# Optimization experiments

Measured on AMD Instinct MI355X. Metric: run time of the kernel, lower is better.

## Reference

```python
import jax, jax.numpy as jnp
import numpy as np


def conv1x1(x, W, b):
    # x: [B,C,H,W], W: [O,C], b: [O]
    return jnp.einsum('bchw,oc->bohw', x, W) + b[None, :, None, None]


def setup_inputs() -> dict:
    key = jax.random.key(0)
    ks = jax.random.split(key, 16)
    B, C, H, W = 4, 256, 64, 64
    C4 = C // 4
    s = lambda fan_in: 1.0 / np.sqrt(fan_in)
    inp = {
        'last_frame': jax.random.normal(ks[0], (B, C, H, W), jnp.float32),
        'current_frame': jax.random.normal(ks[1], (B, C, H, W), jnp.float32),
        'future_frame': jax.random.normal(ks[2], (B, C, H, W), jnp.float32),
        'Wqk': jax.random.normal(ks[3], (C4, C), jnp.float32) * s(C),
        'bqk': jnp.zeros((C4,), jnp.float32),
        'Wkl': jax.random.normal(ks[4], (C4, C), jnp.float32) * s(C),
        'bkl': jnp.zeros((C4,), jnp.float32),
        'Wkf': jax.random.normal(ks[5], (C4, C), jnp.float32) * s(C),
        'bkf': jnp.zeros((C4,), jnp.float32),
        'Wv': jax.random.normal(ks[6], (C4, C), jnp.float32) * s(C),
        'bv': jnp.zeros((C4,), jnp.float32),
        'Wfire': jax.random.normal(ks[7], (C, C // 2), jnp.float32) * s(C // 2),
        'bfire': jnp.zeros((C,), jnp.float32),
        'bn_gamma': jnp.ones((C,), jnp.float32),
        'bn_beta': jnp.zeros((C,), jnp.float32),
        'bn_mean': jnp.zeros((C,), jnp.float32),
        'bn_var': jnp.ones((C,), jnp.float32),
    }
    return inp


def reference(last_frame, current_frame, future_frame,
              Wqk, bqk, Wkl, bkl, Wkf, bkf, Wv, bv,
              Wfire, bfire, bn_gamma, bn_beta, bn_mean, bn_var):
    B, C, H, W = current_frame.shape
    C4 = C // 4
    HW = H * W
    eps = 1e-5

    q = conv1x1(current_frame, Wqk, bqk).reshape(B, C4, HW)       # [B,C4,HW]
    kl = conv1x1(last_frame, Wkl, bkl).reshape(B, C4, HW)          # [B,C4,HW]
    kf = conv1x1(future_frame, Wkf, bkf).reshape(B, C4, HW)        # [B,C4,HW]
    v = conv1x1(current_frame, Wv, bv).reshape(B, C4, HW)          # [B,C4,HW]

    # affinity: [B, HW(query), HW(key)], softmax over key axis
    aff_l = jax.nn.softmax(jnp.einsum('bcq,bck->bqk', q, kl), axis=-1)
    aff_f = jax.nn.softmax(jnp.einsum('bcq,bck->bqk', q, kf), axis=-1)

    # out = V @ A^T : out[b,c,q] = sum_k v[b,c,k] * aff[b,q,k]
    out_l = jnp.einsum('bck,bqk->bcq', v, aff_l).reshape(B, C4, H, W)
    out_f = jnp.einsum('bck,bqk->bcq', v, aff_f).reshape(B, C4, H, W)

    fused = jnp.concatenate([out_l, out_f], axis=1)                 # [B,C/2,H,W]
    fired = conv1x1(fused, Wfire, bfire)                            # [B,C,H,W]
    # BatchNorm (inference form with running stats)
    inv = bn_gamma / jnp.sqrt(bn_var + eps)
    fired = fired * inv[None, :, None, None] + (bn_beta - bn_mean * inv)[None, :, None, None]
    return jax.nn.relu(current_frame + fired)
```

## Files before the change

kernel.cpp:

```cpp
#include <hip/hip_runtime.h>
#include <math.h>
#include <stdint.h>

#define HWN 4096
#define CIN 256
#define CQ 64
#define LOG2E 1.44269504f
#define C2OFF 56.0f

typedef __attribute__((ext_vector_type(8))) _Float16 f16x8;
typedef __attribute__((ext_vector_type(4))) _Float16 f16x4;
typedef __attribute__((ext_vector_type(8))) short    bf16x8;
typedef __attribute__((ext_vector_type(4))) short    bf16x4;
typedef __attribute__((ext_vector_type(4))) float    f32x4;

__device__ __forceinline__ short f2bf(float f) {
  union { float f; uint32_t u; } c; c.f = f;
  uint32_t r = (c.u + 0x7FFFu + ((c.u >> 16) & 1u)) >> 16;
  return (short)(uint16_t)r;
}

__device__ __forceinline__ void stage16(const void* g, void* l) {
  __builtin_amdgcn_global_load_lds(
      (const __attribute__((address_space(1))) uint32_t*)g,
      (__attribute__((address_space(3))) uint32_t*)l, 16, 0, 0);
}

__device__ __forceinline__ void pswap32(uint32_t& a, uint32_t& b) {
  asm volatile("v_permlane32_swap_b32 %0, %1" : "+v"(a), "+v"(b));
}
__device__ __forceinline__ void pswap16(uint32_t& a, uint32_t& b) {
  asm volatile("v_permlane16_swap_b32 %0, %1" : "+v"(a), "+v"(b));
}

__global__ __launch_bounds__(256) void prep_kernel(
    const float* __restrict__ Wqk, const float* __restrict__ Wkl,
    const float* __restrict__ Wkf, const float* __restrict__ Wv,
    const float* __restrict__ Wfire, const float* __restrict__ bfire,
    const float* __restrict__ gamma, const float* __restrict__ beta,
    const float* __restrict__ mean,  const float* __restrict__ var,
    _Float16* __restrict__ wqk_h, _Float16* __restrict__ wkl_h,
    _Float16* __restrict__ wkf_h, _Float16* __restrict__ wv_h,
    _Float16* __restrict__ wf_h, float* __restrict__ scale, float* __restrict__ shift) {
  int gid = blockIdx.x * 256 + threadIdx.x;
  if (gid < CQ * CIN) {
    wqk_h[gid] = (_Float16)(Wqk[gid] * LOG2E);
    wkl_h[gid] = (_Float16)Wkl[gid];
    wkf_h[gid] = (_Float16)Wkf[gid];
    wv_h[gid]  = (_Float16)Wv[gid];
  }
  if (gid < CIN * 128) wf_h[gid] = (_Float16)Wfire[gid];
  if (gid < CIN) {
    float inv = gamma[gid] / sqrtf(var[gid] + 1e-5f);
    scale[gid] = inv;
    shift[gid] = (bfire[gid] - mean[gid]) * inv + beta[gid];
  }
}

__global__ __launch_bounds__(256, 3) void proj_kernel(
    const float* __restrict__ cur, const float* __restrict__ last, const float* __restrict__ fut,
    const _Float16* __restrict__ wqk, const float* __restrict__ bqk,
    const _Float16* __restrict__ wkl, const float* __restrict__ bkl,
    const _Float16* __restrict__ wkf, const float* __restrict__ bkf,
    const _Float16* __restrict__ wv,  const float* __restrict__ bv,
    _Float16* __restrict__ q_out, _Float16* __restrict__ kl_out,
    _Float16* __restrict__ kf_out, short* __restrict__ v_out) {
  const int tid  = threadIdx.x;
  const int w    = tid >> 6;
  const int lane = tid & 63;
  const int quad = lane >> 4;
  const int l15  = lane & 15;
  const int pass = blockIdx.x >> 8;
  const int bb   = blockIdx.x & 255;
  const int b    = bb >> 6;
  const int hwt  = (bb & 63) << 6;
  const int hw   = hwt + w * 16 + l15;

  __shared__ __align__(16) _Float16 Tl[4][16][72];

  const float* X = (pass == 0) ? cur : ((pass == 1) ? last : fut);
  const float* xp = X + (size_t)b * CIN * HWN + hw;

  float xb[8][8];
#pragma unroll
  for (int c0 = 0; c0 < 8; ++c0)
#pragma unroll
    for (int j = 0; j < 8; ++j)
      xb[c0][j] = xp[(size_t)(c0 * 32 + quad * 8 + j) * HWN];

  if (pass == 0) {
    f32x4 aq[4] = {}; f32x4 av[4] = {};
#pragma unroll
    for (int k0 = 0; k0 < 8; ++k0) {
      f16x8 bh;
#pragma unroll
      for (int j = 0; j < 8; ++j) bh[j] = (_Float16)xb[k0][j];
#pragma unroll
      for (int mt = 0; mt < 4; ++mt) {
        f16x8 wa = *(const f16x8*)(wqk + (mt * 16 + l15) * CIN + k0 * 32 + quad * 8);
        aq[mt] = __builtin_amdgcn_mfma_f32_16x16x32_f16(wa, bh, aq[mt], 0, 0, 0);
        f16x8 wb = *(const f16x8*)(wv + (mt * 16 + l15) * CIN + k0 * 32 + quad * 8);
        av[mt] = __builtin_amdgcn_mfma_f32_16x16x32_f16(wb, bh, av[mt], 0, 0, 0);
      }
    }
#pragma unroll
    for (int mt = 0; mt < 4; ++mt)
#pragma unroll
      for (int r = 0; r < 4; ++r) {
        int oc = mt * 16 + quad * 4 + r;
        q_out[((size_t)b * CQ + oc) * HWN + hw] = (_Float16)(aq[mt][r] + bqk[oc] * LOG2E);
        v_out[((size_t)b * CQ + oc) * HWN + hw] = f2bf(av[mt][r] + bv[oc]);
      }
  } else {
    const _Float16* W = (pass == 1) ? wkl : wkf;
    const float* BI = (pass == 1) ? bkl : bkf;
    _Float16* OUT = (pass == 1) ? kl_out : kf_out;
    f32x4 a[4] = {};
#pragma unroll
    for (int k0 = 0; k0 < 8; ++k0) {
      f16x8 bh;
#pragma unroll
      for (int j = 0; j < 8; ++j) bh[j] = (_Float16)xb[k0][j];
#pragma unroll
      for (int mt = 0; mt < 4; ++mt) {
        f16x8 wa = *(const f16x8*)(W + (mt * 16 + l15) * CIN + k0 * 32 + quad * 8);
        a[mt] = __builtin_amdgcn_mfma_f32_16x16x32_f16(wa, bh, a[mt], 0, 0, 0);
      }
    }
#pragma unroll
    for (int mt = 0; mt < 4; ++mt) {
      f16x4 pw;
#pragma unroll
      for (int r = 0; r < 4; ++r)
        pw[r] = (_Float16)(a[mt][r] + BI[mt * 16 + quad * 4 + r]);
      *(f16x4*)&Tl[w][l15][mt * 16 + quad * 4] = pw;
    }
#pragma unroll
    for (int kk = 0; kk < 2; ++kk) {
      f16x8 row = *(const f16x8*)&Tl[w][l15][kk * 32 + quad * 8];
      *(f16x8*)(OUT + ((size_t)b * HWN + hw) * CQ + kk * 32 + quad * 8) = row;
    }
  }
}

__global__ __launch_bounds__(256, 2) void attn_kernel(
    const _Float16* __restrict__ qbuf, const _Float16* __restrict__ klbuf,
    const _Float16* __restrict__ kfbuf, const short* __restrict__ vbuf,
    _Float16* __restrict__ fused) {
  const int tid  = threadIdx.x;
  const int w    = tid >> 6;
  const int lane = tid & 63;
  const int quad = lane >> 4;
  const int l15  = lane & 15;

  const int xcd  = blockIdx.x & 7;
  const int L    = xcd * 64 + (blockIdx.x >> 3);
  const int qt   = (L & 63) << 6;
  const int pair = (L >> 6) & 1;
  const int b    = L >> 7;

  const int kh = w >> 1;
  const int wq = w & 1;

  const _Float16* K  = (pair ? kfbuf : klbuf) + (size_t)b * HWN * CQ;
  const short*    Vg = vbuf + (size_t)b * CQ * HWN;

  __shared__ __align__(16) _Float16 Kt[2][2][64][64];
  __shared__ __align__(16) short    Vt[2][2][64][64];

  const int qbase = qt + wq * 32;
  f16x8 qfrag[2][2];
#pragma unroll
  for (int qg = 0; qg < 2; ++qg)
#pragma unroll
    for (int kk = 0; kk < 2; ++kk)
#pragma unroll
      for (int j = 0; j < 8; ++j)
        qfrag[qg][kk][j] = qbuf[(b * CQ + kk * 32 + quad * 8 + j) * HWN +
                                qbase + qg * 16 + l15];

  f32x4 Oacc[2][4] = {};
  float psum[2] = {0.f, 0.f};

  const int swz  = (lane & 7) ^ ((lane >> 3) & 7);
  const int rswz = l15 & 7;

  const _Float16* ksrc =
      K + ((size_t)(kh * 2048) + wq * 32 + (lane >> 3)) * CQ + swz * 8;
  const short* vsrcS =
      Vg + (size_t)(wq * 32 + (lane >> 3)) * HWN + kh * 2048 + swz * 8;

  auto stageK = [&](int buf, int t) {
#pragma unroll
    for (int r = 0; r < 4; ++r)
      stage16(ksrc + ((size_t)t * 64 + r * 8) * CQ,
              &Kt[buf][kh][wq * 32 + r * 8][0]);
  };
  auto stageV = [&](int buf, int t) {
#pragma unroll
    for (int r = 0; r < 4; ++r)
      stage16(vsrcS + (size_t)(r * 8) * HWN + t * 64,
              &Vt[buf][kh][wq * 32 + r * 8][0]);
  };

  auto body = [&](int buf) {
    f16x8 kf[4][2];
#pragma unroll
    for (int nt = 0; nt < 4; ++nt)
#pragma unroll
      for (int kk = 0; kk < 2; ++kk)
        kf[nt][kk] = *(const f16x8*)&Kt[buf][kh][nt * 16 + l15][((kk * 4 + quad) ^ rswz) * 8];
    bf16x8 vf[4][2];
#pragma unroll
    for (int ct = 0; ct < 4; ++ct)
#pragma unroll
      for (int kk = 0; kk < 2; ++kk)
        vf[ct][kk] = *(const bf16x8*)&Vt[buf][kh][ct * 16 + l15][((kk * 4 + quad) ^ rswz) * 8];
#pragma unroll
    for (int qg = 0; qg < 2; ++qg) {
      f32x4 ST[4] = {};
      __builtin_amdgcn_s_setprio(1);
#pragma unroll
      for (int nt = 0; nt < 4; ++nt)
#pragma unroll
        for (int kk = 0; kk < 2; ++kk)
          ST[nt] = __builtin_amdgcn_mfma_f32_16x16x32_f16(kf[nt][kk], qfrag[qg][kk],
                                                          ST[nt], 0, 0, 0);
      __builtin_amdgcn_s_setprio(0);
      uint32_t D[4][2];
#pragma unroll
      for (int nt = 0; nt < 4; ++nt)
#pragma unroll
        for (int e = 0; e < 2; ++e) {
          float p0 = __builtin_amdgcn_exp2f(ST[nt][2 * e]     - C2OFF);
          float p1 = __builtin_amdgcn_exp2f(ST[nt][2 * e + 1] - C2OFF);
          uint32_t u0 = __float_as_uint(p0) & 0xffff0000u;
          uint32_t u1 = __float_as_uint(p1) & 0xffff0000u;
          psum[qg] += __uint_as_float(u0) + __uint_as_float(u1);
          D[nt][e] = (u0 >> 16) | u1;
        }
#pragma unroll
      for (int kk = 0; kk < 2; ++kk) {
        uint32_t pa0, pa1, pa2, pa3;
        {
          uint32_t u = D[2 * kk][0], v = D[2 * kk + 1][0];
          pswap32(u, v); pswap16(u, v);
          pa0 = u; pa2 = v;
        }
        {
          uint32_t u = D[2 * kk][1], v = D[2 * kk + 1][1];
          pswap32(u, v); pswap16(u, v);
          pa1 = u; pa3 = v;
        }
        union { uint32_t u[4]; bf16x8 v8; } P;
        P.u[0] = pa0; P.u[1] = pa1; P.u[2] = pa2; P.u[3] = pa3;
        __builtin_amdgcn_s_setprio(1);
#pragma unroll
        for (int ct = 0; ct < 4; ++ct)
          Oacc[qg][ct] = __builtin_amdgcn_mfma_f32_16x16x32_bf16(P.v8, vf[ct][kk],
                                                                 Oacc[qg][ct], 0, 0, 0);
        __builtin_amdgcn_s_setprio(0);
      }
    }
  };

  stageK(0, 0); stageV(0, 0);
  __syncthreads();
#pragma unroll 1
  for (int tt = 0; tt < 32; tt += 2) {
    stageK(1, tt + 1); stageV(1, tt + 1);
    body(0);
    __syncthreads();
    if (tt + 2 < 32) { stageK(0, tt + 2); stageV(0, tt + 2); }
    body(1);
    __syncthreads();
  }

#pragma unroll
  for (int qg = 0; qg < 2; ++qg) {
    psum[qg] += __shfl_xor(psum[qg], 16);
    psum[qg] += __shfl_xor(psum[qg], 32);
  }

  float* sc = (float*)&Kt[0][0][0][0];
  float* sp = sc + 4096;
  if (kh) {
#pragma unroll
    for (int qg = 0; qg < 2; ++qg) {
#pragma unroll
      for (int ct = 0; ct < 4; ++ct)
        *(f32x4*)&sc[((((wq * 2 + qg) * 4) + ct) << 8) + lane * 4] = Oacc[qg][ct];
      sp[(wq * 2 + qg) * 64 + lane] = psum[qg];
    }
  }
  __syncthreads();
  if (!kh) {
#pragma unroll
    for (int qg = 0; qg < 2; ++qg) {
      psum[qg] += sp[(wq * 2 + qg) * 64 + lane];
#pragma unroll
      for (int ct = 0; ct < 4; ++ct) {
        f32x4 o2 = *(const f32x4*)&sc[((((wq * 2 + qg) * 4) + ct) << 8) + lane * 4];
        Oacc[qg][ct] += o2;
      }
#pragma unroll
      for (int r = 0; r < 4; ++r) {
        float lt = __shfl(psum[qg], quad * 4 + r);
        float invl = __builtin_amdgcn_rcpf(lt);
        int qi = qbase + qg * 16 + quad * 4 + r;
#pragma unroll
        for (int ct = 0; ct < 4; ++ct)
          fused[((size_t)b * HWN + qi) * 128 + pair * 64 + ct * 16 + l15] =
              (_Float16)(Oacc[qg][ct][r] * invl);
      }
    }
  }
}

__global__ __launch_bounds__(256) void fire_kernel(
    const _Float16* __restrict__ fused, const _Float16* __restrict__ wf,
    const float* __restrict__ scale, const float* __restrict__ shift,
    const float* __restrict__ cur, float* __restrict__ out) {
  const int tid  = threadIdx.x;
  const int w    = tid >> 6;
  const int lane = tid & 63;
  const int quad = lane >> 4;
  const int l15  = lane & 15;
  const int g    = blockIdx.x & 3;
  const int bb   = blockIdx.x >> 2;
  const int b    = bb >> 6;
  const int hwt  = (bb & 63) << 6;
  const int hwb  = hwt + w * 16;

  f16x8 bfr[4];
#pragma unroll
  for (int k0 = 0; k0 < 4; ++k0)
    bfr[k0] = *(const f16x8*)(fused + ((size_t)b * HWN + hwb + l15) * 128 + k0 * 32 + quad * 8);

  float curv[4][4];
#pragma unroll
  for (int mt = 0; mt < 4; ++mt)
#pragma unroll
    for (int r = 0; r < 4; ++r)
      curv[mt][r] = cur[((size_t)b * CIN + g * 64 + mt * 16 + quad * 4 + r) * HWN + hwb + l15];

  f32x4 acc[4] = {};
#pragma unroll
  for (int k0 = 0; k0 < 4; ++k0)
#pragma unroll
    for (int mt = 0; mt < 4; ++mt) {
      f16x8 af = *(const f16x8*)(wf + (g * 64 + mt * 16 + l15) * 128 + k0 * 32 + quad * 8);
      acc[mt] = __builtin_amdgcn_mfma_f32_16x16x32_f16(af, bfr[k0], acc[mt], 0, 0, 0);
    }

#pragma unroll
  for (int mt = 0; mt < 4; ++mt)
#pragma unroll
    for (int r = 0; r < 4; ++r) {
      int oc = g * 64 + mt * 16 + quad * 4 + r;
      size_t idx = ((size_t)b * CIN + oc) * HWN + hwb + l15;
      float y = curv[mt][r] + acc[mt][r] * scale[oc] + shift[oc];
      out[idx] = fmaxf(y, 0.f);
    }
}

extern "C" void kernel_launch(void* const* d_in, const int* in_sizes, int n_in,
                              void* d_out, int out_size, void* d_ws, size_t ws_size,
                              hipStream_t stream) {
  const float* last  = (const float*)d_in[0];
  const float* cur   = (const float*)d_in[1];
  const float* fut   = (const float*)d_in[2];
  const float* Wqk   = (const float*)d_in[3];
  const float* bqk   = (const float*)d_in[4];
  const float* Wkl   = (const float*)d_in[5];
  const float* bkl   = (const float*)d_in[6];
  const float* Wkf   = (const float*)d_in[7];
  const float* bkf   = (const float*)d_in[8];
  const float* Wv    = (const float*)d_in[9];
  const float* bv    = (const float*)d_in[10];
  const float* Wfire = (const float*)d_in[11];
  const float* bfire = (const float*)d_in[12];
  const float* gamma = (const float*)d_in[13];
  const float* beta  = (const float*)d_in[14];
  const float* mean  = (const float*)d_in[15];
  const float* var   = (const float*)d_in[16];

  char* ws = (char*)d_ws;
  _Float16* qb     = (_Float16*)(ws);
  _Float16* klb    = (_Float16*)(ws + (2u << 20));
  _Float16* kfb    = (_Float16*)(ws + (4u << 20));
  short*    vb     = (short*)   (ws + (6u << 20));
  _Float16* fusedb = (_Float16*)(ws + (8u << 20));
  char* wsm = ws + (12u << 20);
  _Float16* wqk_h = (_Float16*)(wsm);
  _Float16* wkl_h = (_Float16*)(wsm + (32u << 10));
  _Float16* wkf_h = (_Float16*)(wsm + (64u << 10));
  _Float16* wv_h  = (_Float16*)(wsm + (96u << 10));
  _Float16* wf_h  = (_Float16*)(wsm + (128u << 10));
  float*    scale = (float*)   (wsm + (192u << 10));
  float*    shift = (float*)   (wsm + (193u << 10));
  float*    out   = (float*)d_out;

  prep_kernel<<<128, 256, 0, stream>>>(Wqk, Wkl, Wkf, Wv, Wfire, bfire,
                                       gamma, beta, mean, var,
                                       wqk_h, wkl_h, wkf_h, wv_h, wf_h, scale, shift);
  proj_kernel<<<768, 256, 0, stream>>>(cur, last, fut, wqk_h, bqk, wkl_h, bkl,
                                       wkf_h, bkf, wv_h, bv, qb, klb, kfb, vb);
  attn_kernel<<<512, 256, 0, stream>>>(qb, klb, kfb, vb, fusedb);
  fire_kernel<<<1024, 256, 0, stream>>>(fusedb, wf_h, scale, shift, cur, out);
}
```

Baseline: 196.5 us.

## Stage projection inputs through double-buffered LDS with async global_load_lds

The projection kernel used to load all 64 input values per thread straight from global memory into registers up front. It now streams each 32-channel slice through a double-buffered shared-memory tile using async global-to-LDS loads, prefetching the next slice while the MFMAs run on the current one. The q/v and k paths are merged into one loop that uses a shared accumulator. This is meant to cut register pressure and overlap memory latency with compute, at the cost of a block barrier per slice and extra LDS reads with a transposed access pattern.

New measurement: 194.9 us. Within noise of the previous version (-0.8%).

```diff
diff --git a/kernel.cpp b/kernel.cpp
--- a/kernel.cpp
+++ b/kernel.cpp
@@ -76,63 +76,69 @@
   const int hwt  = (bb & 63) << 6;
   const int hw   = hwt + w * 16 + l15;
 
+  __shared__ __align__(16) float    Xs[2][8][260];
   __shared__ __align__(16) _Float16 Tl[4][16][72];
 
   const float* X = (pass == 0) ? cur : ((pass == 1) ? last : fut);
-  const float* xp = X + (size_t)b * CIN * HWN + hw;
-
-  float xb[8][8];
-#pragma unroll
-  for (int c0 = 0; c0 < 8; ++c0)
-#pragma unroll
-    for (int j = 0; j < 8; ++j)
-      xb[c0][j] = xp[(size_t)(c0 * 32 + quad * 8 + j) * HWN];
+  const float* xb0 = X + (size_t)b * CIN * HWN + hwt;
+
+  auto stageX = [&](int buf, int cc) {
+#pragma unroll
+    for (int i = 0; i < 2; ++i)
+      stage16(xb0 + (size_t)(cc * 32 + w * 8 + i * 4 + (lane >> 3) / 2) * HWN +
+                  ((lane & 15) << 2),
+              &Xs[buf][w * 2 + i][0]);
+  };
+
+  const _Float16* W1 = (pass == 0) ? wqk : ((pass == 1) ? wkl : wkf);
+  f32x4 a1[4] = {};
+  f32x4 a2[4] = {};
+
+  stageX(0, 0);
+  __syncthreads();
+#pragma unroll 1
+  for (int cc = 0; cc < 8; ++cc) {
+    const int buf = cc & 1;
+    if (cc + 1 < 8) stageX(buf ^ 1, cc + 1);
+    f16x8 bh;
+#pragma unroll
+    for (int j = 0; j < 8; ++j) {
+      const int g = quad * 2 + (j >> 2);
+      bh[j] = (_Float16)Xs[buf][g][(j & 3) * 64 + w * 16 + l15];
+    }
+#pragma unroll
+    for (int mt = 0; mt < 4; ++mt) {
+      f16x8 wa = *(const f16x8*)(W1 + (mt * 16 + l15) * CIN + cc * 32 + quad * 8);
+      a1[mt] = __builtin_amdgcn_mfma_f32_16x16x32_f16(wa, bh, a1[mt], 0, 0, 0);
+    }
+    if (pass == 0) {
+#pragma unroll
+      for (int mt = 0; mt < 4; ++mt) {
+        f16x8 wb = *(const f16x8*)(wv + (mt * 16 + l15) * CIN + cc * 32 + quad * 8);
+        a2[mt] = __builtin_amdgcn_mfma_f32_16x16x32_f16(wb, bh, a2[mt], 0, 0, 0);
+      }
+    }
+    __syncthreads();
+  }
 
   if (pass == 0) {
-    f32x4 aq[4] = {}; f32x4 av[4] = {};
-#pragma unroll
-    for (int k0 = 0; k0 < 8; ++k0) {
-      f16x8 bh;
-#pragma unroll
-      for (int j = 0; j < 8; ++j) bh[j] = (_Float16)xb[k0][j];
-#pragma unroll
-      for (int mt = 0; mt < 4; ++mt) {
-        f16x8 wa = *(const f16x8*)(wqk + (mt * 16 + l15) * CIN + k0 * 32 + quad * 8);
-        aq[mt] = __builtin_amdgcn_mfma_f32_16x16x32_f16(wa, bh, aq[mt], 0, 0, 0);
-        f16x8 wb = *(const f16x8*)(wv + (mt * 16 + l15) * CIN + k0 * 32 + quad * 8);
-        av[mt] = __builtin_amdgcn_mfma_f32_16x16x32_f16(wb, bh, av[mt], 0, 0, 0);
-      }
-    }
 #pragma unroll
     for (int mt = 0; mt < 4; ++mt)
 #pragma unroll
       for (int r = 0; r < 4; ++r) {
         int oc = mt * 16 + quad * 4 + r;
-        q_out[((size_t)b * CQ + oc) * HWN + hw] = (_Float16)(aq[mt][r] + bqk[oc] * LOG2E);
-        v_out[((size_t)b * CQ + oc) * HWN + hw] = f2bf(av[mt][r] + bv[oc]);
+        q_out[((size_t)b * CQ + oc) * HWN + hw] = (_Float16)(a1[mt][r] + bqk[oc] * LOG2E);
+        v_out[((size_t)b * CQ + oc) * HWN + hw] = f2bf(a2[mt][r] + bv[oc]);
       }
   } else {
-    const _Float16* W = (pass == 1) ? wkl : wkf;
     const float* BI = (pass == 1) ? bkl : bkf;
     _Float16* OUT = (pass == 1) ? kl_out : kf_out;
-    f32x4 a[4] = {};
-#pragma unroll
-    for (int k0 = 0; k0 < 8; ++k0) {
-      f16x8 bh;
-#pragma unroll
-      for (int j = 0; j < 8; ++j) bh[j] = (_Float16)xb[k0][j];
-#pragma unroll
-      for (int mt = 0; mt < 4; ++mt) {
-        f16x8 wa = *(const f16x8*)(W + (mt * 16 + l15) * CIN + k0 * 32 + quad * 8);
-        a[mt] = __builtin_amdgcn_mfma_f32_16x16x32_f16(wa, bh, a[mt], 0, 0, 0);
-      }
-    }
 #pragma unroll
     for (int mt = 0; mt < 4; ++mt) {
       f16x4 pw;
 #pragma unroll
       for (int r = 0; r < 4; ++r)
-        pw[r] = (_Float16)(a[mt][r] + BI[mt * 16 + quad * 4 + r]);
+        pw[r] = (_Float16)(a1[mt][r] + BI[mt * 16 + quad * 4 + r]);
       *(f16x4*)&Tl[w][l15][mt * 16 + quad * 4] = pw;
     }
 #pragma unroll
```
